# Optimization experiments

Measured on AMD Instinct MI355X. Metric: run time of the kernel, lower is better.

## Reference

```python
import jax, jax.numpy as jnp
import numpy as np


def setup_inputs() -> dict:
    key = jax.random.key(0)
    x = jax.random.normal(key, (128, 256, 32, 32), dtype=jnp.float32)
    return {"x": x, "iter_num": 5}


def reference(x, iter_num):
    # x: (B, C, H, W)
    B, C, H, W = x.shape
    N = H * W
    xr = x.reshape(B, C, N)
    # Covariance pooling: X @ I_hat @ X^T == (1/N) * Xc @ Xc^T  (I_hat = I/N - J/N^2)
    xc = xr - xr.mean(axis=2, keepdims=True)
    cov = jnp.einsum('bcn,bdn->bcd', xc, xc) / N  # (B, C, C)

    # Newton-Schulz iterative matrix square root
    I = jnp.eye(C, dtype=x.dtype)
    I3 = 3.0 * I
    trace = jnp.trace(cov, axis1=1, axis2=2)[:, None, None]  # norm_A = tr(cov)
    A = cov / trace
    ZY = 0.5 * (I3 - A)
    Y = A @ ZY
    Z = ZY
    for _ in range(1, iter_num - 1):
        ZY = 0.5 * (I3 - Z @ Y)
        Y = Y @ ZY
        Z = ZY @ Z
    YZY = 0.5 * (Y @ (I3 - Z @ Y))
    sqrtm = YZY * jnp.sqrt(trace)  # (B, C, C)

    # Upper-triangular vectorization (row-major, including diagonal)
    r, c = np.triu_indices(C)
    idx = jnp.asarray(r * C + c)
    return sqrtm.reshape(B, C * C)[:, idx]  # (B, C*(C+1)//2)
```

## Files before the change

kernel.cpp:

```cpp
#include <hip/hip_runtime.h>
#include <hip/hip_fp16.h>


typedef _Float16 half8 __attribute__((ext_vector_type(8)));
typedef _Float16 half4 __attribute__((ext_vector_type(4)));
typedef float f32x4 __attribute__((ext_vector_type(4)));

#define OUTPB 32896

__device__ __forceinline__ void gl_lds16(const void* g, void* l) {
  __builtin_amdgcn_global_load_lds(
      (const __attribute__((address_space(1))) void*)g,
      (__attribute__((address_space(3))) void*)l, 16, 0, 0);
}

#define VMB(N) asm volatile("s_waitcnt vmcnt(" #N ")\n\ts_barrier" ::: "memory")
#define LKB()  asm volatile("s_waitcnt lgkmcnt(0)\n\ts_barrier" ::: "memory")

__device__ __forceinline__ void tile_pq(int t, int& p, int& q) {
  p = (t > 3) + (t > 6) + (t > 8);
  int base = p * 4 - (p * (p - 1)) / 2;
  q = p + (t - base);
}

__device__ __forceinline__ half8 cvt8(float4 a, float4 b) {
  half8 h;
  h[0] = (_Float16)a.x; h[1] = (_Float16)a.y; h[2] = (_Float16)a.z; h[3] = (_Float16)a.w;
  h[4] = (_Float16)b.x; h[5] = (_Float16)b.y; h[6] = (_Float16)b.z; h[7] = (_Float16)b.w;
  return h;
}

__device__ __forceinline__ void mfma64(const _Float16* lA, const _Float16* lB,
                                       f32x4 (&acc)[2][2], int wr, int wc,
                                       int lr, int lk) {
#pragma unroll
  for (int ks = 0; ks < 2; ++ks) {
    half8 af[2], bf[2];
#pragma unroll
    for (int m = 0; m < 2; ++m) {
      int row = wr * 32 + m * 16 + lr;
      int kc = (ks * 4 + lk) ^ (row & 7);
      af[m] = *(const half8*)&lA[row * 64 + kc * 8];
    }
#pragma unroll
    for (int n = 0; n < 2; ++n) {
      int row = wc * 32 + n * 16 + lr;
      int kc = (ks * 4 + lk) ^ (row & 7);
      bf[n] = *(const half8*)&lB[row * 64 + kc * 8];
    }
    __builtin_amdgcn_s_setprio(1);
#pragma unroll
    for (int m = 0; m < 2; ++m)
#pragma unroll
      for (int n = 0; n < 2; ++n)
        acc[m][n] = __builtin_amdgcn_mfma_f32_16x16x32_f16(af[m], bf[n], acc[m][n], 0, 0, 0);
    __builtin_amdgcn_s_setprio(0);
  }
}

template <typename F>
__device__ __forceinline__ void store_sym(F f, _Float16* D, size_t boff, int p, int q,
    bool mirror, _Float16* ldsT, f32x4 (&acc)[2][2],
    int wr, int wc, int lr, int lk, int tid) {
#pragma unroll
  for (int m = 0; m < 2; ++m)
#pragma unroll
    for (int n = 0; n < 2; ++n) {
      int il0 = wr * 32 + m * 16 + lk * 4;
      int jl = wc * 32 + n * 16 + lr;
      half4 v4;
#pragma unroll
      for (int r = 0; r < 4; ++r) {
        _Float16 v = f(acc[m][n][r], p * 64 + il0 + r, q * 64 + jl);
        v4[r] = v;
        if (mirror) ldsT[(il0 + r) * 64 + (jl ^ (((il0 + r) & 7) << 3))] = v;
      }
      *(half4*)&D[boff + (size_t)(q * 64 + jl) * 256 + p * 64 + il0] = v4;
    }
  if (mirror) {
    __syncthreads();
#pragma unroll
    for (int pp = 0; pp < 2; ++pp) {
      int u = pp * 256 + tid;
      int im = u >> 3, cu = u & 7;
      half8 v8 = *(const half8*)&ldsT[im * 64 + ((cu ^ (im & 7)) << 3)];
      *(half8*)&D[boff + (size_t)(p * 64 + im) * 256 + q * 64 + cu * 8] = v8;
    }
  }
}

__global__ __launch_bounds__(256, 2) void k_cov(const float* __restrict__ x,
                                                _Float16* __restrict__ covh,
                                                float* __restrict__ trPart) {
  __shared__ _Float16 lds[32768];
  __shared__ float sred[4];

  const int lin = blockIdx.x + 3 * blockIdx.y;
  const int cid = (lin & 7) * 48 + (lin >> 3);
  const int b = cid / 3, t = cid - 3 * b;
  const int p = (t == 1), q = (t != 0);
  const bool diag = (t < 2);
  const int tid = threadIdx.x, w = tid >> 6, lane = tid & 63;
  const int wr = w >> 1, wc = w & 1, lr = lane & 15, lk = lane >> 4;

  const float* Ab = x + ((size_t)b * 256 + p * 128) * 1024;
  const float* Bb = x + ((size_t)b * 256 + q * 128) * 1024;

  float4 la[4][2], lb[4][2];
  f32x4 acc[4][4] = {};
  f32x4 rsA[4] = {}, rsB[4] = {};
  half8 ones;
#pragma unroll
  for (int i = 0; i < 8; ++i) ones[i] = (_Float16)1.0f;

  auto LOAD = [&](int kk) {
#pragma unroll
    for (int i = 0; i < 4; ++i) {
      int u = i * 256 + tid;
      int row = u >> 3, c8 = u & 7;
      int kc = c8 ^ (row & 7);
      const float* sa = Ab + (size_t)row * 1024 + kk * 64 + kc * 8;
      la[i][0] = *(const float4*)sa; la[i][1] = *(const float4*)(sa + 4);
      if (!diag) {
        const float* sb = Bb + (size_t)row * 1024 + kk * 64 + kc * 8;
        lb[i][0] = *(const float4*)sb; lb[i][1] = *(const float4*)(sb + 4);
      }
    }
  };
  auto WRITE = [&](int buf) {
#pragma unroll
    for (int i = 0; i < 4; ++i) {
      int u = i * 256 + tid;
      *(half8*)&lds[buf * 8192 + u * 8] = cvt8(la[i][0], la[i][1]);
      if (!diag) *(half8*)&lds[16384 + buf * 8192 + u * 8] = cvt8(lb[i][0], lb[i][1]);
    }
  };
  auto STEP = [&](const _Float16* lA, const _Float16* lB) {
#pragma unroll
    for (int ks = 0; ks < 2; ++ks) {
      half8 af[4], bf[4];
#pragma unroll
      for (int m = 0; m < 4; ++m) {
        int row = wr * 64 + m * 16 + lr;
        int kc = (ks * 4 + lk) ^ (row & 7);
        af[m] = *(const half8*)&lA[row * 64 + kc * 8];
      }
#pragma unroll
      for (int n = 0; n < 4; ++n) {
        int row = wc * 64 + n * 16 + lr;
        int kc = (ks * 4 + lk) ^ (row & 7);
        bf[n] = *(const half8*)&lB[row * 64 + kc * 8];
      }
      __builtin_amdgcn_s_setprio(1);
#pragma unroll
      for (int m = 0; m < 4; ++m)
        rsA[m] = __builtin_amdgcn_mfma_f32_16x16x32_f16(af[m], ones, rsA[m], 0, 0, 0);
#pragma unroll
      for (int n = 0; n < 4; ++n)
        rsB[n] = __builtin_amdgcn_mfma_f32_16x16x32_f16(ones, bf[n], rsB[n], 0, 0, 0);
#pragma unroll
      for (int m = 0; m < 4; ++m)
#pragma unroll
        for (int n = 0; n < 4; ++n)
          acc[m][n] = __builtin_amdgcn_mfma_f32_16x16x32_f16(af[m], bf[n], acc[m][n], 0, 0, 0);
      __builtin_amdgcn_s_setprio(0);
    }
  };

  LOAD(0); WRITE(0); LOAD(1);
  __syncthreads();
#pragma unroll 1
  for (int kk = 0; kk < 16; ++kk) {
    int cur = kk & 1;
    STEP(&lds[cur * 8192], diag ? &lds[cur * 8192] : &lds[16384 + cur * 8192]);
    if (kk < 15) {
      WRITE(cur ^ 1);
      if (kk < 14) LOAD(kk + 2);
    }
    __syncthreads();
  }

  const float inv = 1.f / 1024.f;
  if (diag) {
    float tp = 0.f;
#pragma unroll
    for (int m = 0; m < 4; ++m)
#pragma unroll
      for (int n = 0; n < 4; ++n)
#pragma unroll
        for (int r = 0; r < 4; ++r) {
          int il = wr * 64 + m * 16 + lk * 4 + r, jl = wc * 64 + n * 16 + lr;
          if (il == jl) tp += (acc[m][n][r] - rsA[m][r] * rsB[n][0] * inv) * inv;
        }
#pragma unroll
    for (int o = 32; o; o >>= 1) tp += __shfl_down(tp, o);
    if (lane == 0) sred[w] = tp;
    __syncthreads();
    if (tid == 0) trPart[b * 2 + p] = sred[0] + sred[1] + sred[2] + sred[3];
  }

  const size_t boff = (size_t)b * 65536;
#pragma unroll
  for (int m = 0; m < 4; ++m)
#pragma unroll
    for (int n = 0; n < 4; ++n) {
      int il0 = wr * 64 + m * 16 + lk * 4;
      int jl = wc * 64 + n * 16 + lr;
      half4 v4;
#pragma unroll
      for (int r = 0; r < 4; ++r) {
        int il = il0 + r;
        float cv = (acc[m][n][r] - rsA[m][r] * rsB[n][0] * inv) * inv;
        v4[r] = (_Float16)cv;
        if (!diag) lds[il * 128 + (((jl >> 3) ^ (il & 7)) << 3) + (jl & 7)] = v4[r];
      }
      *(half4*)&covh[boff + (size_t)(q * 128 + jl) * 256 + p * 128 + il0] = v4;
    }
  if (!diag) {
    __syncthreads();
#pragma unroll
    for (int pp = 0; pp < 8; ++pp) {
      int u = pp * 256 + tid;
      int im = u >> 4, cu = u & 15;
      half8 v8 = *(const half8*)&lds[im * 128 + ((cu ^ (im & 7)) << 3)];
      *(half8*)&covh[boff + (size_t)(p * 128 + im) * 256 + q * 128 + cu * 8] = v8;
    }
  }
}

enum { EPI_S2 = 0, EPI_ZY = 1, EPI_OUT = 2 };

struct GP {
  const _Float16 *A0, *B0;
  _Float16 *D0, *D1;
  const _Float16* covh;
  const float* trP;
  float* outF;
};

template <int EPI>
__global__ __launch_bounds__(256, 4) void k_gemm(GP g) {
  __shared__ _Float16 lds[16384];

  const int lin = blockIdx.x + 10 * blockIdx.y;
  const int cid = (lin & 7) * 160 + (lin >> 3);
  const int b = cid / 10, t = cid - 10 * b;
  int p, q; tile_pq(t, p, q);
  const bool diag = (p == q);
  const bool share = diag && (EPI == EPI_S2);
  const int tid = threadIdx.x, w = tid >> 6, lane = tid & 63;
  const int wr = w >> 1, wc = w & 1, lr = lane & 15, lk = lane >> 4;

  const size_t boff = (size_t)b * 65536;
  const _Float16* Ap = g.A0 + boff + (size_t)p * 64 * 256;
  const _Float16* Bp = ((EPI == EPI_S2) ? g.A0 : g.B0) + boff + (size_t)q * 64 * 256;

  f32x4 acc[2][2] = {};

  auto stageH = [&](const _Float16* panel, int buf, int base, int kk) {
#pragma unroll
    for (int i = 0; i < 2; ++i) {
      int s = (w * 2 + i) * 64 + lane;
      int row = s >> 3, cst = s & 7;
      int kc = cst ^ (row & 7);
      gl_lds16(panel + (size_t)row * 256 + kk * 64 + kc * 8,
               &lds[base + buf * 4096 + (w * 2 + i) * 512]);
    }
  };

  stageH(Ap, 0, 0, 0);
  if (!share) stageH(Bp, 0, 8192, 0);
#pragma unroll 1
  for (int kk = 0; kk < 4; ++kk) {
    int cur = kk & 1;
    if (kk < 3) {
      stageH(Ap, cur ^ 1, 0, kk + 1);
      if (!share) {
        stageH(Bp, cur ^ 1, 8192, kk + 1);
        VMB(4);
      } else {
        VMB(2);
      }
    } else {
      VMB(0);
    }
    mfma64(&lds[cur * 4096], share ? &lds[cur * 4096] : &lds[8192 + cur * 4096],
           acc, wr, wc, lr, lk);
    LKB();
  }

  if constexpr (EPI == EPI_ZY) {
    store_sym([&](float a, int i, int j) {
                return (_Float16)((i == j ? 1.5f : 0.f) - 0.5f * a);
              }, g.D0, boff, p, q, !diag, lds, acc, wr, wc, lr, lk, tid);
  } else if constexpr (EPI == EPI_S2) {
    float tv = g.trP[b * 2] + g.trP[b * 2 + 1];
    float it1 = 1.f / tv;
    _Float16* TY = lds;
    _Float16* TZ = lds + 4096;
#pragma unroll
    for (int m = 0; m < 2; ++m)
#pragma unroll
      for (int n = 0; n < 2; ++n) {
        int il0 = wr * 32 + m * 16 + lk * 4;
        int jl = wc * 32 + n * 16 + lr;
        half4 c4 = *(const half4*)&g.covh[boff + (size_t)(q * 64 + jl) * 256 + p * 64 + il0];
        half4 y4, z4;
#pragma unroll
        for (int r = 0; r < 4; ++r) {
          int i = p * 64 + il0 + r, j = q * 64 + jl;
          float c = (float)c4[r];
          y4[r] = (_Float16)(1.5f * c * it1 - 0.5f * acc[m][n][r] * it1 * it1);
          z4[r] = (_Float16)((i == j ? 1.5f : 0.f) - 0.5f * c * it1);
          if (!diag) {
            int sp = (il0 + r) * 64 + (jl ^ (((il0 + r) & 7) << 3));
            TY[sp] = y4[r]; TZ[sp] = z4[r];
          }
        }
        *(half4*)&g.D0[boff + (size_t)(q * 64 + jl) * 256 + p * 64 + il0] = y4;
        *(half4*)&g.D1[boff + (size_t)(q * 64 + jl) * 256 + p * 64 + il0] = z4;
      }
    if (!diag) {
      __syncthreads();
#pragma unroll
      for (int pp = 0; pp < 2; ++pp) {
        int u = pp * 256 + tid;
        int im = u >> 3, cu = u & 7;
        half8 vy = *(const half8*)&TY[im * 64 + ((cu ^ (im & 7)) << 3)];
        half8 vz = *(const half8*)&TZ[im * 64 + ((cu ^ (im & 7)) << 3)];
        *(half8*)&g.D0[boff + (size_t)(p * 64 + im) * 256 + q * 64 + cu * 8] = vy;
        *(half8*)&g.D1[boff + (size_t)(p * 64 + im) * 256 + q * 64 + cu * 8] = vz;
      }
    }
  } else {
    float tv = g.trP[b * 2] + g.trP[b * 2 + 1];
    float st = sqrtf(tv);
#pragma unroll
    for (int m = 0; m < 2; ++m)
#pragma unroll
      for (int n = 0; n < 2; ++n)
#pragma unroll
        for (int r = 0; r < 4; ++r) {
          int i = p * 64 + wr * 32 + m * 16 + lk * 4 + r;
          int j = q * 64 + wc * 32 + n * 16 + lr;
          if (i <= j) {
            int idx = j + i * 256 - (i * (i + 1)) / 2;
            g.outF[(size_t)b * OUTPB + idx] = acc[m][n][r] * st;
          }
        }
  }
}

struct YZP {
  const _Float16 *Y, *Z, *W;
  _Float16 *Yn, *Zn;
};

__global__ __launch_bounds__(256, 3) void k_yzm(YZP g) {
  __shared__ _Float16 lds[24576];

  const int lin = blockIdx.x + 10 * blockIdx.y;
  const int cid = (lin & 7) * 160 + (lin >> 3);
  const int b = cid / 10, t = cid - 10 * b;
  int p, q; tile_pq(t, p, q);
  const bool diag = (p == q);
  const int tid = threadIdx.x, w = tid >> 6, lane = tid & 63;
  const int wr = w >> 1, wc = w & 1, lr = lane & 15, lk = lane >> 4;

  const size_t boff = (size_t)b * 65536;
  const _Float16* Yp = g.Y + boff + (size_t)p * 64 * 256;
  const _Float16* Zp = g.Z + boff + (size_t)p * 64 * 256;
  const _Float16* Wp = g.W + boff + (size_t)q * 64 * 256;

  f32x4 accY[2][2] = {}, accZ[2][2] = {};

  auto stageH = [&](const _Float16* panel, int buf, int base, int kk) {
#pragma unroll
    for (int i = 0; i < 2; ++i) {
      int s = (w * 2 + i) * 64 + lane;
      int row = s >> 3, cst = s & 7;
      int kc = cst ^ (row & 7);
      gl_lds16(panel + (size_t)row * 256 + kk * 64 + kc * 8,
               &lds[base + buf * 4096 + (w * 2 + i) * 512]);
    }
  };

  auto step = [&](const _Float16* lY, const _Float16* lZ, const _Float16* lW) {
#pragma unroll
    for (int ks = 0; ks < 2; ++ks) {
      half8 yf[2], zf[2], wf[2];
#pragma unroll
      for (int m = 0; m < 2; ++m) {
        int row = wr * 32 + m * 16 + lr;
        int kc = (ks * 4 + lk) ^ (row & 7);
        yf[m] = *(const half8*)&lY[row * 64 + kc * 8];
        zf[m] = *(const half8*)&lZ[row * 64 + kc * 8];
      }
#pragma unroll
      for (int n = 0; n < 2; ++n) {
        int row = wc * 32 + n * 16 + lr;
        int kc = (ks * 4 + lk) ^ (row & 7);
        wf[n] = *(const half8*)&lW[row * 64 + kc * 8];
      }
      __builtin_amdgcn_s_setprio(1);
#pragma unroll
      for (int m = 0; m < 2; ++m)
#pragma unroll
        for (int n = 0; n < 2; ++n) {
          accY[m][n] = __builtin_amdgcn_mfma_f32_16x16x32_f16(yf[m], wf[n], accY[m][n], 0, 0, 0);
          accZ[m][n] = __builtin_amdgcn_mfma_f32_16x16x32_f16(zf[m], wf[n], accZ[m][n], 0, 0, 0);
        }
      __builtin_amdgcn_s_setprio(0);
    }
  };

  stageH(Yp, 0, 0, 0); stageH(Zp, 0, 8192, 0); stageH(Wp, 0, 16384, 0);
#pragma unroll 1
  for (int kk = 0; kk < 4; ++kk) {
    int cur = kk & 1;
    if (kk < 3) {
      stageH(Yp, cur ^ 1, 0, kk + 1);
      stageH(Zp, cur ^ 1, 8192, kk + 1);
      stageH(Wp, cur ^ 1, 16384, kk + 1);
      VMB(6);
    } else {
      VMB(0);
    }
    step(&lds[cur * 4096], &lds[8192 + cur * 4096], &lds[16384 + cur * 4096]);
    LKB();
  }

  _Float16* TY = lds;
  _Float16* TZ = lds + 4096;
#pragma unroll
  for (int m = 0; m < 2; ++m)
#pragma unroll
    for (int n = 0; n < 2; ++n) {
      int il0 = wr * 32 + m * 16 + lk * 4;
      int jl = wc * 32 + n * 16 + lr;
      half4 y4, z4;
#pragma unroll
      for (int r = 0; r < 4; ++r) {
        y4[r] = (_Float16)accY[m][n][r];
        z4[r] = (_Float16)accZ[m][n][r];
        if (!diag) {
          int sp = (il0 + r) * 64 + (jl ^ (((il0 + r) & 7) << 3));
          TY[sp] = y4[r]; TZ[sp] = z4[r];
        }
      }
      *(half4*)&g.Yn[boff + (size_t)(q * 64 + jl) * 256 + p * 64 + il0] = y4;
      *(half4*)&g.Zn[boff + (size_t)(q * 64 + jl) * 256 + p * 64 + il0] = z4;
    }
  if (!diag) {
    __syncthreads();
#pragma unroll
    for (int pp = 0; pp < 2; ++pp) {
      int u = pp * 256 + tid;
      int im = u >> 3, cu = u & 7;
      half8 vy = *(const half8*)&TY[im * 64 + ((cu ^ (im & 7)) << 3)];
      half8 vz = *(const half8*)&TZ[im * 64 + ((cu ^ (im & 7)) << 3)];
      *(half8*)&g.Yn[boff + (size_t)(p * 64 + im) * 256 + q * 64 + cu * 8] = vy;
      *(half8*)&g.Zn[boff + (size_t)(p * 64 + im) * 256 + q * 64 + cu * 8] = vz;
    }
  }
}

extern "C" void kernel_launch(void* const* d_in, const int* in_sizes, int n_in,
                              void* d_out, int out_size, void* d_ws, size_t ws_size,
                              hipStream_t stream) {
  const float* x = (const float*)d_in[0];
  float* outF = (float*)d_out;

  char* ws = (char*)d_ws;
  const size_t MATB = (size_t)128 * 65536 * sizeof(_Float16);
  _Float16* covh = (_Float16*)ws;
  _Float16* Y0   = (_Float16*)(ws + MATB);
  _Float16* Z0   = (_Float16*)(ws + 2 * MATB);
  _Float16* Y1   = (_Float16*)(ws + 3 * MATB);
  _Float16* Z1   = (_Float16*)(ws + 4 * MATB);
  float* trP     = (float*)(ws + 5 * MATB);

  dim3 g3(3, 128), g10(10, 128);

  k_cov<<<g3, 256, 0, stream>>>(x, covh, trP);

  {
    GP a{};
    a.A0 = covh; a.D0 = Y0; a.D1 = Z0;
    a.covh = covh; a.trP = trP;
    k_gemm<EPI_S2><<<g10, 256, 0, stream>>>(a);
  }

  _Float16 *Yc = Y0, *Zc = Z0, *Yn = Y1, *Zn = Z1;
  for (int itn = 0; itn < 3; ++itn) {
    GP a{};
    a.A0 = Zc; a.B0 = Yc; a.D0 = covh;
    k_gemm<EPI_ZY><<<g10, 256, 0, stream>>>(a);
    YZP r{};
    r.Y = Yc; r.Z = Zc; r.W = covh; r.Yn = Yn; r.Zn = Zn;
    k_yzm<<<g10, 256, 0, stream>>>(r);
    _Float16* t0 = Yc; Yc = Yn; Yn = t0;
    _Float16* t1 = Zc; Zc = Zn; Zn = t1;
  }
  {
    GP a{};
    a.A0 = Zc; a.B0 = Yc; a.D0 = covh;
    k_gemm<EPI_ZY><<<g10, 256, 0, stream>>>(a);
    GP o{};
    o.A0 = Yc; o.B0 = covh; o.trP = trP; o.outF = outF;
    k_gemm<EPI_OUT><<<g10, 256, 0, stream>>>(o);
  }
}
```

Before: 159.0 us.

## Fuse Newton-Schulz stages into persistent kernel with per-batch dataflow counters

```diff
diff --git a/kernel.cpp b/kernel.cpp
--- a/kernel.cpp
+++ b/kernel.cpp
@@ -89,173 +89,9 @@
   }
 }
 
-__global__ __launch_bounds__(256, 2) void k_cov(const float* __restrict__ x,
-                                                _Float16* __restrict__ covh,
-                                                float* __restrict__ trPart) {
-  __shared__ _Float16 lds[32768];
-  __shared__ float sred[4];
-
-  const int lin = blockIdx.x + 3 * blockIdx.y;
-  const int cid = (lin & 7) * 48 + (lin >> 3);
-  const int b = cid / 3, t = cid - 3 * b;
-  const int p = (t == 1), q = (t != 0);
-  const bool diag = (t < 2);
-  const int tid = threadIdx.x, w = tid >> 6, lane = tid & 63;
-  const int wr = w >> 1, wc = w & 1, lr = lane & 15, lk = lane >> 4;
-
-  const float* Ab = x + ((size_t)b * 256 + p * 128) * 1024;
-  const float* Bb = x + ((size_t)b * 256 + q * 128) * 1024;
-
-  float4 la[4][2], lb[4][2];
-  f32x4 acc[4][4] = {};
-  f32x4 rsA[4] = {}, rsB[4] = {};
-  half8 ones;
-#pragma unroll
-  for (int i = 0; i < 8; ++i) ones[i] = (_Float16)1.0f;
-
-  auto LOAD = [&](int kk) {
-#pragma unroll
-    for (int i = 0; i < 4; ++i) {
-      int u = i * 256 + tid;
-      int row = u >> 3, c8 = u & 7;
-      int kc = c8 ^ (row & 7);
-      const float* sa = Ab + (size_t)row * 1024 + kk * 64 + kc * 8;
-      la[i][0] = *(const float4*)sa; la[i][1] = *(const float4*)(sa + 4);
-      if (!diag) {
-        const float* sb = Bb + (size_t)row * 1024 + kk * 64 + kc * 8;
-        lb[i][0] = *(const float4*)sb; lb[i][1] = *(const float4*)(sb + 4);
-      }
-    }
-  };
-  auto WRITE = [&](int buf) {
-#pragma unroll
-    for (int i = 0; i < 4; ++i) {
-      int u = i * 256 + tid;
-      *(half8*)&lds[buf * 8192 + u * 8] = cvt8(la[i][0], la[i][1]);
-      if (!diag) *(half8*)&lds[16384 + buf * 8192 + u * 8] = cvt8(lb[i][0], lb[i][1]);
-    }
-  };
-  auto STEP = [&](const _Float16* lA, const _Float16* lB) {
-#pragma unroll
-    for (int ks = 0; ks < 2; ++ks) {
-      half8 af[4], bf[4];
-#pragma unroll
-      for (int m = 0; m < 4; ++m) {
-        int row = wr * 64 + m * 16 + lr;
-        int kc = (ks * 4 + lk) ^ (row & 7);
-        af[m] = *(const half8*)&lA[row * 64 + kc * 8];
-      }
-#pragma unroll
-      for (int n = 0; n < 4; ++n) {
-        int row = wc * 64 + n * 16 + lr;
-        int kc = (ks * 4 + lk) ^ (row & 7);
-        bf[n] = *(const half8*)&lB[row * 64 + kc * 8];
-      }
-      __builtin_amdgcn_s_setprio(1);
-#pragma unroll
-      for (int m = 0; m < 4; ++m)
-        rsA[m] = __builtin_amdgcn_mfma_f32_16x16x32_f16(af[m], ones, rsA[m], 0, 0, 0);
-#pragma unroll
-      for (int n = 0; n < 4; ++n)
-        rsB[n] = __builtin_amdgcn_mfma_f32_16x16x32_f16(ones, bf[n], rsB[n], 0, 0, 0);
-#pragma unroll
-      for (int m = 0; m < 4; ++m)
-#pragma unroll
-        for (int n = 0; n < 4; ++n)
-          acc[m][n] = __builtin_amdgcn_mfma_f32_16x16x32_f16(af[m], bf[n], acc[m][n], 0, 0, 0);
-      __builtin_amdgcn_s_setprio(0);
-    }
-  };
-
-  LOAD(0); WRITE(0); LOAD(1);
-  __syncthreads();
-#pragma unroll 1
-  for (int kk = 0; kk < 16; ++kk) {
-    int cur = kk & 1;
-    STEP(&lds[cur * 8192], diag ? &lds[cur * 8192] : &lds[16384 + cur * 8192]);
-    if (kk < 15) {
-      WRITE(cur ^ 1);
-      if (kk < 14) LOAD(kk + 2);
-    }
-    __syncthreads();
-  }
-
-  const float inv = 1.f / 1024.f;
-  if (diag) {
-    float tp = 0.f;
-#pragma unroll
-    for (int m = 0; m < 4; ++m)
-#pragma unroll
-      for (int n = 0; n < 4; ++n)
-#pragma unroll
-        for (int r = 0; r < 4; ++r) {
-          int il = wr * 64 + m * 16 + lk * 4 + r, jl = wc * 64 + n * 16 + lr;
-          if (il == jl) tp += (acc[m][n][r] - rsA[m][r] * rsB[n][0] * inv) * inv;
-        }
-#pragma unroll
-    for (int o = 32; o; o >>= 1) tp += __shfl_down(tp, o);
-    if (lane == 0) sred[w] = tp;
-    __syncthreads();
-    if (tid == 0) trPart[b * 2 + p] = sred[0] + sred[1] + sred[2] + sred[3];
-  }
-
-  const size_t boff = (size_t)b * 65536;
-#pragma unroll
-  for (int m = 0; m < 4; ++m)
-#pragma unroll
-    for (int n = 0; n < 4; ++n) {
-      int il0 = wr * 64 + m * 16 + lk * 4;
-      int jl = wc * 64 + n * 16 + lr;
-      half4 v4;
-#pragma unroll
-      for (int r = 0; r < 4; ++r) {
-        int il = il0 + r;
-        float cv = (acc[m][n][r] - rsA[m][r] * rsB[n][0] * inv) * inv;
-        v4[r] = (_Float16)cv;
-        if (!diag) lds[il * 128 + (((jl >> 3) ^ (il & 7)) << 3) + (jl & 7)] = v4[r];
-      }
-      *(half4*)&covh[boff + (size_t)(q * 128 + jl) * 256 + p * 128 + il0] = v4;
-    }
-  if (!diag) {
-    __syncthreads();
-#pragma unroll
-    for (int pp = 0; pp < 8; ++pp) {
-      int u = pp * 256 + tid;
-      int im = u >> 4, cu = u & 15;
-      half8 v8 = *(const half8*)&lds[im * 128 + ((cu ^ (im & 7)) << 3)];
-      *(half8*)&covh[boff + (size_t)(p * 128 + im) * 256 + q * 128 + cu * 8] = v8;
-    }
-  }
-}
-
-enum { EPI_S2 = 0, EPI_ZY = 1, EPI_OUT = 2 };
-
-struct GP {
-  const _Float16 *A0, *B0;
-  _Float16 *D0, *D1;
-  const _Float16* covh;
-  const float* trP;
-  float* outF;
-};
-
-template <int EPI>
-__global__ __launch_bounds__(256, 4) void k_gemm(GP g) {
-  __shared__ _Float16 lds[16384];
-
-  const int lin = blockIdx.x + 10 * blockIdx.y;
-  const int cid = (lin & 7) * 160 + (lin >> 3);
-  const int b = cid / 10, t = cid - 10 * b;
-  int p, q; tile_pq(t, p, q);
-  const bool diag = (p == q);
-  const bool share = diag && (EPI == EPI_S2);
-  const int tid = threadIdx.x, w = tid >> 6, lane = tid & 63;
-  const int wr = w >> 1, wc = w & 1, lr = lane & 15, lk = lane >> 4;
-
-  const size_t boff = (size_t)b * 65536;
-  const _Float16* Ap = g.A0 + boff + (size_t)p * 64 * 256;
-  const _Float16* Bp = ((EPI == EPI_S2) ? g.A0 : g.B0) + boff + (size_t)q * 64 * 256;
-
-  f32x4 acc[2][2] = {};
+__device__ __forceinline__ void gemm64(const _Float16* Ap, const _Float16* Bp,
+    bool share, _Float16* lds, f32x4 (&acc)[2][2], int tid) {
+  const int w = tid >> 6, lane = tid & 63;
 
   auto stageH = [&](const _Float16* panel, int buf, int base, int kk) {
 #pragma unroll
@@ -268,6 +104,7 @@
     }
   };
 
+  const int wr = w >> 1, wc = w & 1, lr = lane & 15, lk = lane >> 4;
   stageH(Ap, 0, 0, 0);
   if (!share) stageH(Bp, 0, 8192, 0);
 #pragma unroll 1
@@ -288,90 +125,88 @@
            acc, wr, wc, lr, lk);
     LKB();
   }
-
-  if constexpr (EPI == EPI_ZY) {
-    store_sym([&](float a, int i, int j) {
-                return (_Float16)((i == j ? 1.5f : 0.f) - 0.5f * a);
-              }, g.D0, boff, p, q, !diag, lds, acc, wr, wc, lr, lk, tid);
-  } else if constexpr (EPI == EPI_S2) {
-    float tv = g.trP[b * 2] + g.trP[b * 2 + 1];
-    float it1 = 1.f / tv;
-    _Float16* TY = lds;
-    _Float16* TZ = lds + 4096;
-#pragma unroll
-    for (int m = 0; m < 2; ++m)
-#pragma unroll
-      for (int n = 0; n < 2; ++n) {
-        int il0 = wr * 32 + m * 16 + lk * 4;
-        int jl = wc * 32 + n * 16 + lr;
-        half4 c4 = *(const half4*)&g.covh[boff + (size_t)(q * 64 + jl) * 256 + p * 64 + il0];
-        half4 y4, z4;
-#pragma unroll
-        for (int r = 0; r < 4; ++r) {
-          int i = p * 64 + il0 + r, j = q * 64 + jl;
-          float c = (float)c4[r];
-          y4[r] = (_Float16)(1.5f * c * it1 - 0.5f * acc[m][n][r] * it1 * it1);
-          z4[r] = (_Float16)((i == j ? 1.5f : 0.f) - 0.5f * c * it1);
-          if (!diag) {
-            int sp = (il0 + r) * 64 + (jl ^ (((il0 + r) & 7) << 3));
-            TY[sp] = y4[r]; TZ[sp] = z4[r];
-          }
-        }
-        *(half4*)&g.D0[boff + (size_t)(q * 64 + jl) * 256 + p * 64 + il0] = y4;
-        *(half4*)&g.D1[boff + (size_t)(q * 64 + jl) * 256 + p * 64 + il0] = z4;
-      }
-    if (!diag) {
-      __syncthreads();
-#pragma unroll
-      for (int pp = 0; pp < 2; ++pp) {
-        int u = pp * 256 + tid;
-        int im = u >> 3, cu = u & 7;
-        half8 vy = *(const half8*)&TY[im * 64 + ((cu ^ (im & 7)) << 3)];
-        half8 vz = *(const half8*)&TZ[im * 64 + ((cu ^ (im & 7)) << 3)];
-        *(half8*)&g.D0[boff + (size_t)(p * 64 + im) * 256 + q * 64 + cu * 8] = vy;
-        *(half8*)&g.D1[boff + (size_t)(p * 64 + im) * 256 + q * 64 + cu * 8] = vz;
-      }
-    }
-  } else {
-    float tv = g.trP[b * 2] + g.trP[b * 2 + 1];
-    float st = sqrtf(tv);
-#pragma unroll
-    for (int m = 0; m < 2; ++m)
-#pragma unroll
-      for (int n = 0; n < 2; ++n)
-#pragma unroll
-        for (int r = 0; r < 4; ++r) {
-          int i = p * 64 + wr * 32 + m * 16 + lk * 4 + r;
-          int j = q * 64 + wc * 32 + n * 16 + lr;
-          if (i <= j) {
-            int idx = j + i * 256 - (i * (i + 1)) / 2;
-            g.outF[(size_t)b * OUTPB + idx] = acc[m][n][r] * st;
-          }
-        }
-  }
-}
-
-struct YZP {
-  const _Float16 *Y, *Z, *W;
-  _Float16 *Yn, *Zn;
-};
-
-__global__ __launch_bounds__(256, 3) void k_yzm(YZP g) {
-  __shared__ _Float16 lds[24576];
-
-  const int lin = blockIdx.x + 10 * blockIdx.y;
-  const int cid = (lin & 7) * 160 + (lin >> 3);
-  const int b = cid / 10, t = cid - 10 * b;
+}
+
+__device__ __forceinline__ void run_s2(int b, int t, const _Float16* covh,
+    const float* trP, _Float16* Y0, _Float16* Z0, _Float16* lds, int tid) {
   int p, q; tile_pq(t, p, q);
   const bool diag = (p == q);
-  const int tid = threadIdx.x, w = tid >> 6, lane = tid & 63;
+  const int w = tid >> 6, lane = tid & 63;
   const int wr = w >> 1, wc = w & 1, lr = lane & 15, lk = lane >> 4;
-
   const size_t boff = (size_t)b * 65536;
-  const _Float16* Yp = g.Y + boff + (size_t)p * 64 * 256;
-  const _Float16* Zp = g.Z + boff + (size_t)p * 64 * 256;
-  const _Float16* Wp = g.W + boff + (size_t)q * 64 * 256;
-
+
+  f32x4 acc[2][2] = {};
+  gemm64(covh + boff + (size_t)p * 64 * 256, covh + boff + (size_t)q * 64 * 256,
+         diag, lds, acc, tid);
+
+  float tv = trP[b * 2] + trP[b * 2 + 1];
+  float it1 = 1.f / tv;
+  _Float16* TY = lds;
+  _Float16* TZ = lds + 4096;
+#pragma unroll
+  for (int m = 0; m < 2; ++m)
+#pragma unroll
+    for (int n = 0; n < 2; ++n) {
+      int il0 = wr * 32 + m * 16 + lk * 4;
+      int jl = wc * 32 + n * 16 + lr;
+      half4 c4 = *(const half4*)&covh[boff + (size_t)(q * 64 + jl) * 256 + p * 64 + il0];
+      half4 y4, z4;
+#pragma unroll
+      for (int r = 0; r < 4; ++r) {
+        int i = p * 64 + il0 + r, j = q * 64 + jl;
+        float c = (float)c4[r];
+        y4[r] = (_Float16)(1.5f * c * it1 - 0.5f * acc[m][n][r] * it1 * it1);
+        z4[r] = (_Float16)((i == j ? 1.5f : 0.f) - 0.5f * c * it1);
+        if (!diag) {
+          int sp = (il0 + r) * 64 + (jl ^ (((il0 + r) & 7) << 3));
+          TY[sp] = y4[r]; TZ[sp] = z4[r];
+        }
+      }
+      *(half4*)&Y0[boff + (size_t)(q * 64 + jl) * 256 + p * 64 + il0] = y4;
+      *(half4*)&Z0[boff + (size_t)(q * 64 + jl) * 256 + p * 64 + il0] = z4;
+    }
+  if (!diag) {
+    __syncthreads();
+#pragma unroll
+    for (int pp = 0; pp < 2; ++pp) {
+      int u = pp * 256 + tid;
+      int im = u >> 3, cu = u & 7;
+      half8 vy = *(const half8*)&TY[im * 64 + ((cu ^ (im & 7)) << 3)];
+      half8 vz = *(const half8*)&TZ[im * 64 + ((cu ^ (im & 7)) << 3)];
+      *(half8*)&Y0[boff + (size_t)(p * 64 + im) * 256 + q * 64 + cu * 8] = vy;
+      *(half8*)&Z0[boff + (size_t)(p * 64 + im) * 256 + q * 64 + cu * 8] = vz;
+    }
+  }
+}
+
+__device__ __forceinline__ void run_v(int b, int t, const _Float16* Z,
+    const _Float16* Y, _Float16* W, _Float16* lds, int tid) {
+  int p, q; tile_pq(t, p, q);
+  const bool diag = (p == q);
+  const int w = tid >> 6, lane = tid & 63;
+  const int wr = w >> 1, wc = w & 1, lr = lane & 15, lk = lane >> 4;
+  const size_t boff = (size_t)b * 65536;
+
+  f32x4 acc[2][2] = {};
+  gemm64(Z + boff + (size_t)p * 64 * 256, Y + boff + (size_t)q * 64 * 256,
+         false, lds, acc, tid);
+  store_sym([&](float a, int i, int j) {
+              return (_Float16)((i == j ? 1.5f : 0.f) - 0.5f * a);
+            }, W, boff, p, q, !diag, lds, acc, wr, wc, lr, lk, tid);
+}
+
+__device__ __forceinline__ void run_yz(int b, int t, const _Float16* Y,
+    const _Float16* Z, const _Float16* W, _Float16* Yn, _Float16* Zn,
+    _Float16* lds, int tid) {
+  int p, q; tile_pq(t, p, q);
+  const bool diag = (p == q);
+  const int w = tid >> 6, lane = tid & 63;
+  const int wr = w >> 1, wc = w & 1, lr = lane & 15, lk = lane >> 4;
+  const size_t boff = (size_t)b * 65536;
+
+  const _Float16* Yp = Y + boff + (size_t)p * 64 * 256;
+  const _Float16* Zp = Z + boff + (size_t)p * 64 * 256;
+  const _Float16* Wp = W + boff + (size_t)q * 64 * 256;
   f32x4 accY[2][2] = {}, accZ[2][2] = {};
 
   auto stageH = [&](const _Float16* panel, int buf, int base, int kk) {
@@ -384,7 +219,6 @@
                &lds[base + buf * 4096 + (w * 2 + i) * 512]);
     }
   };
-
   auto step = [&](const _Float16* lY, const _Float16* lZ, const _Float16* lW) {
 #pragma unroll
     for (int ks = 0; ks < 2; ++ks) {
@@ -448,8 +282,8 @@
           TY[sp] = y4[r]; TZ[sp] = z4[r];
         }
       }
-      *(half4*)&g.Yn[boff + (size_t)(q * 64 + jl) * 256 + p * 64 + il0] = y4;
-      *(half4*)&g.Zn[boff + (size_t)(q * 64 + jl) * 256 + p * 64 + il0] = z4;
+      *(half4*)&Yn[boff + (size_t)(q * 64 + jl) * 256 + p * 64 + il0] = y4;
+      *(half4*)&Zn[boff + (size_t)(q * 64 + jl) * 256 + p * 64 + il0] = z4;
     }
   if (!diag) {
     __syncthreads();
@@ -459,10 +293,252 @@
       int im = u >> 3, cu = u & 7;
       half8 vy = *(const half8*)&TY[im * 64 + ((cu ^ (im & 7)) << 3)];
       half8 vz = *(const half8*)&TZ[im * 64 + ((cu ^ (im & 7)) << 3)];
-      *(half8*)&g.Yn[boff + (size_t)(p * 64 + im) * 256 + q * 64 + cu * 8] = vy;
-      *(half8*)&g.Zn[boff + (size_t)(p * 64 + im) * 256 + q * 64 + cu * 8] = vz;
-    }
-  }
+      *(half8*)&Yn[boff + (size_t)(p * 64 + im) * 256 + q * 64 + cu * 8] = vy;
+      *(half8*)&Zn[boff + (size_t)(p * 64 + im) * 256 + q * 64 + cu * 8] = vz;
+    }
+  }
+}
+
+__device__ __forceinline__ void run_out(int b, int t, const _Float16* Y,
+    const _Float16* W, const float* trP, float* outF, _Float16* lds, int tid) {
+  int p, q; tile_pq(t, p, q);
+  const int w = tid >> 6, lane = tid & 63;
+  const int wr = w >> 1, wc = w & 1, lr = lane & 15, lk = lane >> 4;
+  const size_t boff = (size_t)b * 65536;
+
+  f32x4 acc[2][2] = {};
+  gemm64(Y + boff + (size_t)p * 64 * 256, W + boff + (size_t)q * 64 * 256,
+         false, lds, acc, tid);
+  float tv = trP[b * 2] + trP[b * 2 + 1];
+  float st = sqrtf(tv);
+#pragma unroll
+  for (int m = 0; m < 2; ++m)
+#pragma unroll
+    for (int n = 0; n < 2; ++n)
+#pragma unroll
+      for (int r = 0; r < 4; ++r) {
+        int i = p * 64 + wr * 32 + m * 16 + lk * 4 + r;
+        int j = q * 64 + wc * 32 + n * 16 + lr;
+        if (i <= j) {
+          int idx = j + i * 256 - (i * (i + 1)) / 2;
+          outF[(size_t)b * OUTPB + idx] = acc[m][n][r] * st;
+        }
+      }
+}
+
+__global__ __launch_bounds__(256, 2) void k_cov(const float* __restrict__ x,
+                                                _Float16* __restrict__ covh,
+                                                float* __restrict__ trPart) {
+  __shared__ _Float16 lds[32768];
+  __shared__ float sred[4];
+
+  const int lin = blockIdx.x + 3 * blockIdx.y;
+  const int cid = (lin & 7) * 48 + (lin >> 3);
+  const int b = cid / 3, t = cid - 3 * b;
+  const int p = (t == 1), q = (t != 0);
+  const bool diag = (t < 2);
+  const int tid = threadIdx.x, w = tid >> 6, lane = tid & 63;
+  const int wr = w >> 1, wc = w & 1, lr = lane & 15, lk = lane >> 4;
+
+  const float* Ab = x + ((size_t)b * 256 + p * 128) * 1024;
+  const float* Bb = x + ((size_t)b * 256 + q * 128) * 1024;
+
+  float4 la[4][2], lb[4][2];
+  f32x4 acc[4][4] = {};
+  f32x4 rsA[4] = {}, rsB[4] = {};
+  half8 ones;
+#pragma unroll
+  for (int i = 0; i < 8; ++i) ones[i] = (_Float16)1.0f;
+
+  auto LOAD = [&](int kk) {
+#pragma unroll
+    for (int i = 0; i < 4; ++i) {
+      int u = i * 256 + tid;
+      int row = u >> 3, c8 = u & 7;
+      int kc = c8 ^ (row & 7);
+      const float* sa = Ab + (size_t)row * 1024 + kk * 64 + kc * 8;
+      la[i][0] = *(const float4*)sa; la[i][1] = *(const float4*)(sa + 4);
+      if (!diag) {
+        const float* sb = Bb + (size_t)row * 1024 + kk * 64 + kc * 8;
+        lb[i][0] = *(const float4*)sb; lb[i][1] = *(const float4*)(sb + 4);
+      }
+    }
+  };
+  auto WRITE = [&](int buf) {
+#pragma unroll
+    for (int i = 0; i < 4; ++i) {
+      int u = i * 256 + tid;
+      *(half8*)&lds[buf * 8192 + u * 8] = cvt8(la[i][0], la[i][1]);
+      if (!diag) *(half8*)&lds[16384 + buf * 8192 + u * 8] = cvt8(lb[i][0], lb[i][1]);
+    }
+  };
+  auto STEP = [&](const _Float16* lA, const _Float16* lB) {
+#pragma unroll
+    for (int ks = 0; ks < 2; ++ks) {
+      half8 af[4], bf[4];
+#pragma unroll
+      for (int m = 0; m < 4; ++m) {
+        int row = wr * 64 + m * 16 + lr;
+        int kc = (ks * 4 + lk) ^ (row & 7);
+        af[m] = *(const half8*)&lA[row * 64 + kc * 8];
+      }
+#pragma unroll
+      for (int n = 0; n < 4; ++n) {
+        int row = wc * 64 + n * 16 + lr;
+        int kc = (ks * 4 + lk) ^ (row & 7);
+        bf[n] = *(const half8*)&lB[row * 64 + kc * 8];
+      }
+      __builtin_amdgcn_s_setprio(1);
+#pragma unroll
+      for (int m = 0; m < 4; ++m)
+        rsA[m] = __builtin_amdgcn_mfma_f32_16x16x32_f16(af[m], ones, rsA[m], 0, 0, 0);
+#pragma unroll
+      for (int n = 0; n < 4; ++n)
+        rsB[n] = __builtin_amdgcn_mfma_f32_16x16x32_f16(ones, bf[n], rsB[n], 0, 0, 0);
+#pragma unroll
+      for (int m = 0; m < 4; ++m)
+#pragma unroll
+        for (int n = 0; n < 4; ++n)
+          acc[m][n] = __builtin_amdgcn_mfma_f32_16x16x32_f16(af[m], bf[n], acc[m][n], 0, 0, 0);
+      __builtin_amdgcn_s_setprio(0);
+    }
+  };
+
+  LOAD(0); WRITE(0); LOAD(1);
+  __syncthreads();
+#pragma unroll 1
+  for (int kk = 0; kk < 16; ++kk) {
+    int cur = kk & 1;
+    STEP(&lds[cur * 8192], diag ? &lds[cur * 8192] : &lds[16384 + cur * 8192]);
+    if (kk < 15) {
+      WRITE(cur ^ 1);
+      if (kk < 14) LOAD(kk + 2);
+    }
+    __syncthreads();
+  }
+
+  const float inv = 1.f / 1024.f;
+  if (diag) {
+    float tp = 0.f;
+#pragma unroll
+    for (int m = 0; m < 4; ++m)
+#pragma unroll
+      for (int n = 0; n < 4; ++n)
+#pragma unroll
+        for (int r = 0; r < 4; ++r) {
+          int il = wr * 64 + m * 16 + lk * 4 + r, jl = wc * 64 + n * 16 + lr;
+          if (il == jl) tp += (acc[m][n][r] - rsA[m][r] * rsB[n][0] * inv) * inv;
+        }
+#pragma unroll
+    for (int o = 32; o; o >>= 1) tp += __shfl_down(tp, o);
+    if (lane == 0) sred[w] = tp;
+    __syncthreads();
+    if (tid == 0) trPart[b * 2 + p] = sred[0] + sred[1] + sred[2] + sred[3];
+  }
+
+  const size_t boff = (size_t)b * 65536;
+#pragma unroll
+  for (int m = 0; m < 4; ++m)
+#pragma unroll
+    for (int n = 0; n < 4; ++n) {
+      int il0 = wr * 64 + m * 16 + lk * 4;
+      int jl = wc * 64 + n * 16 + lr;
+      half4 v4;
+#pragma unroll
+      for (int r = 0; r < 4; ++r) {
+        int il = il0 + r;
+        float cv = (acc[m][n][r] - rsA[m][r] * rsB[n][0] * inv) * inv;
+        v4[r] = (_Float16)cv;
+        if (!diag) lds[il * 128 + (((jl >> 3) ^ (il & 7)) << 3) + (jl & 7)] = v4[r];
+      }
+      *(half4*)&covh[boff + (size_t)(q * 128 + jl) * 256 + p * 128 + il0] = v4;
+    }
+  if (!diag) {
+    __syncthreads();
+#pragma unroll
+    for (int pp = 0; pp < 8; ++pp) {
+      int u = pp * 256 + tid;
+      int im = u >> 4, cu = u & 15;
+      half8 v8 = *(const half8*)&lds[im * 128 + ((cu ^ (im & 7)) << 3)];
+      *(half8*)&covh[boff + (size_t)(p * 128 + im) * 256 + q * 128 + cu * 8] = v8;
+    }
+  }
+}
+
+struct PP {
+  const _Float16* covh;
+  const float* trP;
+  float* outF;
+  _Float16 *Y1, *Z1, *W1, *Y2, *Z2, *W2, *Y3, *Z3, *W3, *Y4, *Z4, *W4;
+  unsigned* cnt;
+};
+
+__global__ __launch_bounds__(256, 3) void k_pipe(PP P) {
+  __shared__ _Float16 lds[24576];
+  const int tid = threadIdx.x;
+  const int xcd = blockIdx.x & 7, l = blockIdx.x >> 3;
+
+#pragma unroll 1
+  for (int g = l; g < 1440; g += 96) {
+    int s = g / 160, r = g - s * 160;
+    int b = xcd * 16 + r / 10, t = r - 10 * (r / 10);
+
+    if (s > 0) {
+      if (tid == 0) {
+        while (__hip_atomic_load(&P.cnt[b * 16 + s - 1], __ATOMIC_ACQUIRE,
+                                 __HIP_MEMORY_SCOPE_AGENT) < 10u)
+          __builtin_amdgcn_s_sleep(2);
+      }
+      __syncthreads();
+    }
+
+    if (s == 0)      run_s2(b, t, P.covh, P.trP, P.Y1, P.Z1, lds, tid);
+    else if (s == 1) run_v(b, t, P.Z1, P.Y1, P.W1, lds, tid);
+    else if (s == 2) run_yz(b, t, P.Y1, P.Z1, P.W1, P.Y2, P.Z2, lds, tid);
+    else if (s == 3) run_v(b, t, P.Z2, P.Y2, P.W2, lds, tid);
+    else if (s == 4) run_yz(b, t, P.Y2, P.Z2, P.W2, P.Y3, P.Z3, lds, tid);
+    else if (s == 5) run_v(b, t, P.Z3, P.Y3, P.W3, lds, tid);
+    else if (s == 6) run_yz(b, t, P.Y3, P.Z3, P.W3, P.Y4, P.Z4, lds, tid);
+    else if (s == 7) run_v(b, t, P.Z4, P.Y4, P.W4, lds, tid);
+    else             run_out(b, t, P.Y4, P.W4, P.trP, P.outF, lds, tid);
+
+    __threadfence();
+    __syncthreads();
+    if (tid == 0 && s < 8)
+      __hip_atomic_fetch_add(&P.cnt[b * 16 + s], 1u, __ATOMIC_RELEASE,
+                             __HIP_MEMORY_SCOPE_AGENT);
+  }
+}
+
+__device__ __forceinline__ void fb_decode(int& b, int& t) {
+  int lin = blockIdx.x + 10 * blockIdx.y;
+  int cid = (lin & 7) * 160 + (lin >> 3);
+  b = cid / 10; t = cid - 10 * b;
+}
+__global__ __launch_bounds__(256, 4) void k_s2F(const _Float16* covh, const float* trP,
+                                                _Float16* Y0, _Float16* Z0) {
+  __shared__ _Float16 lds[16384];
+  int b, t; fb_decode(b, t);
+  run_s2(b, t, covh, trP, Y0, Z0, lds, threadIdx.x);
+}
+__global__ __launch_bounds__(256, 4) void k_vF(const _Float16* Z, const _Float16* Y,
+                                               _Float16* W) {
+  __shared__ _Float16 lds[16384];
+  int b, t; fb_decode(b, t);
+  run_v(b, t, Z, Y, W, lds, threadIdx.x);
+}
+__global__ __launch_bounds__(256, 3) void k_yzF(const _Float16* Y, const _Float16* Z,
+                                                const _Float16* W, _Float16* Yn,
+                                                _Float16* Zn) {
+  __shared__ _Float16 lds[24576];
+  int b, t; fb_decode(b, t);
+  run_yz(b, t, Y, Z, W, Yn, Zn, lds, threadIdx.x);
+}
+__global__ __launch_bounds__(256, 4) void k_outF(const _Float16* Y, const _Float16* W,
+                                                 const float* trP, float* outF) {
+  __shared__ _Float16 lds[16384];
+  int b, t; fb_decode(b, t);
+  run_out(b, t, Y, W, trP, outF, lds, threadIdx.x);
 }
 
 extern "C" void kernel_launch(void* const* d_in, const int* in_sizes, int n_in,
@@ -473,6 +549,32 @@
 
   char* ws = (char*)d_ws;
   const size_t MATB = (size_t)128 * 65536 * sizeof(_Float16);
+  const size_t NEED = 13 * MATB + 16384;
+
+  dim3 g3(3, 128), g10(10, 128);
+
+  int maxb = 0;
+  hipError_t qe = hipOccupancyMaxActiveBlocksPerMultiprocessor(
+      &maxb, (const void*)k_pipe, 256, 0);
+
+  if (qe == hipSuccess && maxb >= 3 && ws_size >= NEED) {
+    PP P;
+    P.covh = (const _Float16*)ws;
+    _Float16* mats = (_Float16*)(ws + MATB);
+    P.Y1 = mats + 0 * (MATB / 2);  P.Z1 = mats + 1 * (MATB / 2);  P.W1 = mats + 2 * (MATB / 2);
+    P.Y2 = mats + 3 * (MATB / 2);  P.Z2 = mats + 4 * (MATB / 2);  P.W2 = mats + 5 * (MATB / 2);
+    P.Y3 = mats + 6 * (MATB / 2);  P.Z3 = mats + 7 * (MATB / 2);  P.W3 = mats + 8 * (MATB / 2);
+    P.Y4 = mats + 9 * (MATB / 2);  P.Z4 = mats + 10 * (MATB / 2); P.W4 = mats + 11 * (MATB / 2);
+    float* trP = (float*)(ws + 13 * MATB);
+    unsigned* cnt = (unsigned*)(ws + 13 * MATB + 4096);
+    P.trP = trP; P.outF = outF; P.cnt = cnt;
+
+    hipMemsetAsync(cnt, 0, 128 * 16 * sizeof(unsigned), stream);
+    k_cov<<<g3, 256, 0, stream>>>(x, (_Float16*)P.covh, trP);
+    k_pipe<<<dim3(768), 256, 0, stream>>>(P);
+    return;
+  }
+
   _Float16* covh = (_Float16*)ws;
   _Float16* Y0   = (_Float16*)(ws + MATB);
   _Float16* Z0   = (_Float16*)(ws + 2 * MATB);
@@ -480,34 +582,15 @@
   _Float16* Z1   = (_Float16*)(ws + 4 * MATB);
   float* trP     = (float*)(ws + 5 * MATB);
 
-  dim3 g3(3, 128), g10(10, 128);
-
   k_cov<<<g3, 256, 0, stream>>>(x, covh, trP);
-
-  {
-    GP a{};
-    a.A0 = covh; a.D0 = Y0; a.D1 = Z0;
-    a.covh = covh; a.trP = trP;
-    k_gemm<EPI_S2><<<g10, 256, 0, stream>>>(a);
-  }
-
+  k_s2F<<<g10, 256, 0, stream>>>(covh, trP, Y0, Z0);
   _Float16 *Yc = Y0, *Zc = Z0, *Yn = Y1, *Zn = Z1;
   for (int itn = 0; itn < 3; ++itn) {
-    GP a{};
-    a.A0 = Zc; a.B0 = Yc; a.D0 = covh;
-    k_gemm<EPI_ZY><<<g10, 256, 0, stream>>>(a);
-    YZP r{};
-    r.Y = Yc; r.Z = Zc; r.W = covh; r.Yn = Yn; r.Zn = Zn;
-    k_yzm<<<g10, 256, 0, stream>>>(r);
+    k_vF<<<g10, 256, 0, stream>>>(Zc, Yc, covh);
+    k_yzF<<<g10, 256, 0, stream>>>(Yc, Zc, covh, Yn, Zn);
     _Float16* t0 = Yc; Yc = Yn; Yn = t0;
     _Float16* t1 = Zc; Zc = Zn; Zn = t1;
   }
-  {
-    GP a{};
-    a.A0 = Zc; a.B0 = Yc; a.D0 = covh;
-    k_gemm<EPI_ZY><<<g10, 256, 0, stream>>>(a);
-    GP o{};
-    o.A0 = Yc; o.B0 = covh; o.trP = trP; o.outF = outF;
-    k_gemm<EPI_OUT><<<g10, 256, 0, stream>>>(o);
-  }
-}
+  k_vF<<<g10, 256, 0, stream>>>(Zc, Yc, covh);
+  k_outF<<<g10, 256, 0, stream>>>(Yc, covh, trP, outF);
+}
```

Measured after the change: 159.2 us. Within noise of the previous version (+0.1%).
